# Optimization experiments

Hardware: AMD Instinct MI355X
Metric: run time of the kernel (lower is better)

## Reference

```python
import jax, jax.numpy as jnp
import numpy as np

RADIUS = 0.2
NSAMPLE = 32


def setup_inputs() -> dict:
    key = jax.random.key(0)
    k1, k2 = jax.random.split(key)
    B, N = 8, 4096
    xyz = jax.random.uniform(k1, (B, N, 3), dtype=jnp.float32)
    xyz_new = jax.random.uniform(k2, (B, N, 3), dtype=jnp.float32)  # ignored by forward, kept for signature fidelity
    return {"xyz": xyz, "xyz_new": xyz_new}


def _ball_query(radius, nsample, xyz, new_xyz):
    # xyz: [B, N, 3] source points; new_xyz: [B, M, 3] query centers.
    # Returns idx: [B, M, nsample] int32, matching pointnet2 CUDA ball_query:
    # first `nsample` indices j (in increasing j order) with ||q - p_j||^2 < r^2;
    # unused slots are filled with the first valid index.
    B, N, _ = xyz.shape
    sq_src = jnp.sum(xyz * xyz, axis=-1)          # [B, N]
    sq_q = jnp.sum(new_xyz * new_xyz, axis=-1)    # [B, M]
    # d2[b, m, n] = ||q_m - p_n||^2
    d2 = sq_q[:, :, None] + sq_src[:, None, :] - 2.0 * jnp.einsum(
        "bmc,bnc->bmn", new_xyz, xyz)             # [B, M, N]
    mask = d2 < (radius * radius)                 # [B, M, N] bool
    # key = index j when within radius, else sentinel N (sorts to the end)
    idx_range = jnp.arange(N, dtype=jnp.int32)
    keys = jnp.where(mask, idx_range[None, None, :], jnp.int32(N))
    sorted_keys = jnp.sort(keys, axis=-1)[..., :nsample]  # [B, M, nsample]
    first = sorted_keys[..., 0:1]                 # first valid index (pad value)
    idx = jnp.where(sorted_keys < N, sorted_keys, first)
    return idx.astype(jnp.int32)


def reference(xyz, xyz_new):
    # Faithful to the module: ball_query(radius, nsample, xyz, xyz) — xyz_new unused.
    return _ball_query(RADIUS, NSAMPLE, xyz, xyz)
```

## Files before the change

kernel.cpp:

```cpp
#include <hip/hip_runtime.h>
#include <cstdint>


#define BQ_N    4096
#define BQ_HALF 2048
#define BQ_B    8
#define BQ_NS   32
#define BQ_R2   0.04f

__device__ __forceinline__ float sq_plain(float x, float y, float z) {
    float r, t;
    asm("v_mul_f32 %0, %2, %2\n\t"
        "v_mul_f32 %1, %3, %3\n\t"
        "v_add_f32 %0, %0, %1\n\t"
        "v_mul_f32 %1, %4, %4\n\t"
        "v_add_f32 %0, %0, %1"
        : "=&v"(r), "=&v"(t)
        : "v"(x), "v"(y), "v"(z));
    return r;
}

__device__ __forceinline__ float d2_mixed(float qx, float qy, float qz, float sqq,
                                          float sx, float sy, float sz, float sqs) {
    float r, t;
    asm("v_mul_f32 %0, %2, %5\n\t"
        "v_fma_f32 %0, %3, %6, %0\n\t"
        "v_fma_f32 %0, %4, %7, %0\n\t"
        "v_add_f32 %0, %0, %0\n\t"
        "v_add_f32 %1, %8, %9\n\t"
        "v_sub_f32 %0, %1, %0"
        : "=&v"(r), "=&v"(t)
        : "v"(qx), "v"(qy), "v"(qz), "v"(sx), "v"(sy), "v"(sz),
          "v"(sqq), "v"(sqs));
    return r;
}

__device__ __forceinline__ void scan1(const float4* pts, int lane,
                                      const float4& q, int c,
                                      uint64_t& word, int& found) {
    #pragma unroll
    for (int u = 0; u < 4; ++u) {
        const int k = (c << 2) + u;
        const float4 s = pts[((k & 31) << 6) + lane];
        const float d2 = d2_mixed(q.x, q.y, q.z, q.w, s.x, s.y, s.z, s.w);
        const uint64_t bal = __ballot(d2 < BQ_R2);
        if (lane == k) word = bal;
        found += (int)__popcll(bal);
    }
}

__device__ __forceinline__ void scan2(const float4* pts, int lane,
                                      const float4& q0, const float4& q1,
                                      int c0, int c1,
                                      uint64_t& w0, uint64_t& w1,
                                      int& f0, int& f1) {
    int c = c0;
    while (c < c1) {
        #pragma unroll
        for (int u = 0; u < 4; ++u) {
            const int k = (c << 2) + u;
            const float4 s = pts[((k & 31) << 6) + lane];
            const float d20 = d2_mixed(q0.x, q0.y, q0.z, q0.w,
                                       s.x, s.y, s.z, s.w);
            const float d21 = d2_mixed(q1.x, q1.y, q1.z, q1.w,
                                       s.x, s.y, s.z, s.w);
            const uint64_t b0 = __ballot(d20 < BQ_R2);
            const uint64_t b1 = __ballot(d21 < BQ_R2);
            if (lane == k) { w0 = b0; w1 = b1; }
            f0 += (int)__popcll(b0);
            f1 += (int)__popcll(b1);
        }
        ++c;
        if (f0 >= BQ_NS || f1 >= BQ_NS) break;
    }
    for (int ca = c; ca < c1 && f0 < BQ_NS; ++ca) scan1(pts, lane, q0, ca, w0, f0);
    for (int cb = c; cb < c1 && f1 < BQ_NS; ++cb) scan1(pts, lane, q1, cb, w1, f1);
}

__device__ __forceinline__ void emit_query(int* orow, int lane, uint64_t word) {
    const int cnt = __popcll(word);
    int incl = cnt;
    #pragma unroll
    for (int off = 1; off < 64; off <<= 1) {
        const int t = __shfl_up(incl, off);
        if (lane >= off) incl += t;
    }
    const int pre   = incl - cnt;
    const int total = __shfl(incl, 63);

    int first;
    const uint64_t nz = __ballot(word != 0ull);
    if (nz == 0ull) {
        first = BQ_N;
    } else {
        const int fl = __builtin_ctzll(nz);
        const uint64_t fw = __shfl(word, fl);
        first = (fl << 6) + __builtin_ctzll(fw);
    }

    uint64_t w = word;
    int pos = pre;
    while (w != 0ull && pos < BQ_NS) {
        const int bit = __builtin_ctzll(w);
        orow[pos] = (lane << 6) + bit;
        w &= (w - 1);
        ++pos;
    }
    if (lane >= total && lane < BQ_NS) orow[lane] = first;
}

__global__ __launch_bounds__(256, 4)
void ball_query_kernel(const float* __restrict__ xyz, int* __restrict__ out)
{
    __shared__ float4 pts[BQ_HALF];

    const int b     = blockIdx.x >> 7;
    const int qbase = (blockIdx.x & 127) << 5;
    const float* __restrict__ src = xyz + (size_t)b * BQ_N * 3;
    const int lane = threadIdx.x & 63;
    const int wid  = threadIdx.x >> 6;
    int* __restrict__ outb = out + (size_t)(b * BQ_N) * BQ_NS;

    float4 Q[8];
    #pragma unroll
    for (int j = 0; j < 8; ++j) {
        const int m = qbase + (wid << 3) + j;
        const float x = src[3 * m + 0];
        const float y = src[3 * m + 1];
        const float z = src[3 * m + 2];
        Q[j] = make_float4(x, y, z, sq_plain(x, y, z));
    }

    for (int j = threadIdx.x; j < BQ_HALF; j += 256) {
        const float x = src[3 * j + 0];
        const float y = src[3 * j + 1];
        const float z = src[3 * j + 2];
        pts[j] = make_float4(x, y, z, sq_plain(x, y, z));
    }
    __syncthreads();

    uint64_t W[8] = {0, 0, 0, 0, 0, 0, 0, 0};
    int      F[8] = {0, 0, 0, 0, 0, 0, 0, 0};

    #pragma unroll
    for (int p = 0; p < 4; ++p)
        scan2(pts, lane, Q[p], Q[p + 4], 0, 8, W[p], W[p + 4], F[p], F[p + 4]);

    __syncthreads();
    for (int j = threadIdx.x; j < BQ_HALF; j += 256) {
        const int g = BQ_HALF + j;
        const float x = src[3 * g + 0];
        const float y = src[3 * g + 1];
        const float z = src[3 * g + 2];
        pts[j] = make_float4(x, y, z, sq_plain(x, y, z));
    }
    __syncthreads();

    #pragma unroll
    for (int p = 0; p < 4; ++p) {
        if (F[p] < BQ_NS && F[p + 4] < BQ_NS) {
            scan2(pts, lane, Q[p], Q[p + 4], 8, 16,
                  W[p], W[p + 4], F[p], F[p + 4]);
        } else if (F[p] < BQ_NS) {
            for (int ca = 8; ca < 16 && F[p] < BQ_NS; ++ca)
                scan1(pts, lane, Q[p], ca, W[p], F[p]);
        } else if (F[p + 4] < BQ_NS) {
            for (int cb = 8; cb < 16 && F[p + 4] < BQ_NS; ++cb)
                scan1(pts, lane, Q[p + 4], cb, W[p + 4], F[p + 4]);
        }
    }

    #pragma unroll
    for (int j = 0; j < 8; ++j) {
        const int m = qbase + (wid << 3) + j;
        emit_query(outb + (size_t)m * BQ_NS, lane, W[j]);
    }
}

extern "C" void kernel_launch(void* const* d_in, const int* in_sizes, int n_in,
                              void* d_out, int out_size, void* d_ws, size_t ws_size,
                              hipStream_t stream)
{
    const float* xyz = (const float*)d_in[0];
    int* out = (int*)d_out;
    hipLaunchKernelGGL(ball_query_kernel, dim3(1024), dim3(256), 0, stream,
                       xyz, out);
}
```

Measured before the change: 83.71 us.

## Stream source points from global memory and drop shared-memory staging

The shared-memory staging of source points, with its two-phase load and block barriers, is removed. Each wave now reads xyz directly from global memory (relying on L1/L2 caching) and computes squared norms on the fly. Blocks shrink to 128 threads with 4 queries per wave, so more blocks launch. Per-lane prefix counts are recorded during the scan, which removes the shuffle-based prefix sum in emit, and the pad value is computed only when fewer than nsample neighbours were found. The trade-off is strided 3-float global loads and recomputing norms per query pair instead of loading them once into LDS.

```diff
diff --git a/kernel.cpp b/kernel.cpp
--- a/kernel.cpp
+++ b/kernel.cpp
@@ -3,7 +3,6 @@
 
 
 #define BQ_N    4096
-#define BQ_HALF 2048
 #define BQ_B    8
 #define BQ_NS   32
 #define BQ_R2   0.04f
@@ -35,145 +34,117 @@
     return r;
 }
 
-__device__ __forceinline__ void scan1(const float4* pts, int lane,
-                                      const float4& q, int c,
-                                      uint64_t& word, int& found) {
+__device__ __forceinline__ void scan1g(const float* __restrict__ src, int lane,
+                                       const float4& q, int c,
+                                       uint64_t& word, int& wpre, int& found) {
+    float X[4], Y[4], Z[4];
     #pragma unroll
     for (int u = 0; u < 4; ++u) {
         const int k = (c << 2) + u;
-        const float4 s = pts[((k & 31) << 6) + lane];
-        const float d2 = d2_mixed(q.x, q.y, q.z, q.w, s.x, s.y, s.z, s.w);
+        const float* ptr = src + (size_t)(((k << 6) + lane) * 3);
+        X[u] = ptr[0]; Y[u] = ptr[1]; Z[u] = ptr[2];
+    }
+    #pragma unroll
+    for (int u = 0; u < 4; ++u) {
+        const int k = (c << 2) + u;
+        const float sqs = sq_plain(X[u], Y[u], Z[u]);
+        const float d2  = d2_mixed(q.x, q.y, q.z, q.w, X[u], Y[u], Z[u], sqs);
         const uint64_t bal = __ballot(d2 < BQ_R2);
-        if (lane == k) word = bal;
+        if (lane == k) { word = bal; wpre = found; }
         found += (int)__popcll(bal);
     }
 }
 
-__device__ __forceinline__ void scan2(const float4* pts, int lane,
-                                      const float4& q0, const float4& q1,
-                                      int c0, int c1,
-                                      uint64_t& w0, uint64_t& w1,
-                                      int& f0, int& f1) {
+__device__ __forceinline__ void scan2g(const float* __restrict__ src, int lane,
+                                       const float4& q0, const float4& q1,
+                                       int c0, int c1,
+                                       uint64_t& w0, uint64_t& w1,
+                                       int& p0, int& p1, int& f0, int& f1) {
     int c = c0;
     while (c < c1) {
+        float X[4], Y[4], Z[4];
         #pragma unroll
         for (int u = 0; u < 4; ++u) {
             const int k = (c << 2) + u;
-            const float4 s = pts[((k & 31) << 6) + lane];
+            const float* ptr = src + (size_t)(((k << 6) + lane) * 3);
+            X[u] = ptr[0]; Y[u] = ptr[1]; Z[u] = ptr[2];
+        }
+        #pragma unroll
+        for (int u = 0; u < 4; ++u) {
+            const int k = (c << 2) + u;
+            const float sqs = sq_plain(X[u], Y[u], Z[u]);
             const float d20 = d2_mixed(q0.x, q0.y, q0.z, q0.w,
-                                       s.x, s.y, s.z, s.w);
+                                       X[u], Y[u], Z[u], sqs);
             const float d21 = d2_mixed(q1.x, q1.y, q1.z, q1.w,
-                                       s.x, s.y, s.z, s.w);
+                                       X[u], Y[u], Z[u], sqs);
             const uint64_t b0 = __ballot(d20 < BQ_R2);
             const uint64_t b1 = __ballot(d21 < BQ_R2);
-            if (lane == k) { w0 = b0; w1 = b1; }
+            if (lane == k) { w0 = b0; w1 = b1; p0 = f0; p1 = f1; }
             f0 += (int)__popcll(b0);
             f1 += (int)__popcll(b1);
         }
         ++c;
         if (f0 >= BQ_NS || f1 >= BQ_NS) break;
     }
-    for (int ca = c; ca < c1 && f0 < BQ_NS; ++ca) scan1(pts, lane, q0, ca, w0, f0);
-    for (int cb = c; cb < c1 && f1 < BQ_NS; ++cb) scan1(pts, lane, q1, cb, w1, f1);
+    for (int ca = c; ca < c1 && f0 < BQ_NS; ++ca) scan1g(src, lane, q0, ca, w0, p0, f0);
+    for (int cb = c; cb < c1 && f1 < BQ_NS; ++cb) scan1g(src, lane, q1, cb, w1, p1, f1);
 }
 
-__device__ __forceinline__ void emit_query(int* orow, int lane, uint64_t word) {
-    const int cnt = __popcll(word);
-    int incl = cnt;
-    #pragma unroll
-    for (int off = 1; off < 64; off <<= 1) {
-        const int t = __shfl_up(incl, off);
-        if (lane >= off) incl += t;
-    }
-    const int pre   = incl - cnt;
-    const int total = __shfl(incl, 63);
-
-    int first;
-    const uint64_t nz = __ballot(word != 0ull);
-    if (nz == 0ull) {
-        first = BQ_N;
-    } else {
-        const int fl = __builtin_ctzll(nz);
-        const uint64_t fw = __shfl(word, fl);
-        first = (fl << 6) + __builtin_ctzll(fw);
-    }
-
+__device__ __forceinline__ void emit_query(int* __restrict__ orow, int lane,
+                                           uint64_t word, int wpre, int total) {
     uint64_t w = word;
-    int pos = pre;
+    int pos = wpre;
     while (w != 0ull && pos < BQ_NS) {
         const int bit = __builtin_ctzll(w);
         orow[pos] = (lane << 6) + bit;
         w &= (w - 1);
         ++pos;
     }
-    if (lane >= total && lane < BQ_NS) orow[lane] = first;
+    if (total < BQ_NS) {
+        int first;
+        const uint64_t nz = __ballot(word != 0ull);
+        if (nz == 0ull) {
+            first = BQ_N;
+        } else {
+            const int fl = __builtin_ctzll(nz);
+            const uint64_t fw = __shfl(word, fl);
+            first = (fl << 6) + __builtin_ctzll(fw);
+        }
+        if (lane >= total && lane < BQ_NS) orow[lane] = first;
+    }
 }
 
-__global__ __launch_bounds__(256, 4)
+__global__ __launch_bounds__(128, 4)
 void ball_query_kernel(const float* __restrict__ xyz, int* __restrict__ out)
 {
-    __shared__ float4 pts[BQ_HALF];
-
-    const int b     = blockIdx.x >> 7;
-    const int qbase = (blockIdx.x & 127) << 5;
+    const int b     = blockIdx.x >> 9;
+    const int qbase = (blockIdx.x & 511) << 3;
+    const int lane  = threadIdx.x & 63;
+    const int wid   = threadIdx.x >> 6;
     const float* __restrict__ src = xyz + (size_t)b * BQ_N * 3;
-    const int lane = threadIdx.x & 63;
-    const int wid  = threadIdx.x >> 6;
     int* __restrict__ outb = out + (size_t)(b * BQ_N) * BQ_NS;
 
-    float4 Q[8];
+    float4 Q[4];
     #pragma unroll
-    for (int j = 0; j < 8; ++j) {
-        const int m = qbase + (wid << 3) + j;
+    for (int j = 0; j < 4; ++j) {
+        const int m = qbase + (wid << 2) + j;
         const float x = src[3 * m + 0];
         const float y = src[3 * m + 1];
         const float z = src[3 * m + 2];
         Q[j] = make_float4(x, y, z, sq_plain(x, y, z));
     }
 
-    for (int j = threadIdx.x; j < BQ_HALF; j += 256) {
-        const float x = src[3 * j + 0];
-        const float y = src[3 * j + 1];
-        const float z = src[3 * j + 2];
-        pts[j] = make_float4(x, y, z, sq_plain(x, y, z));
-    }
-    __syncthreads();
+    uint64_t W[4] = {0, 0, 0, 0};
+    int      P[4] = {0, 0, 0, 0};
+    int      F[4] = {0, 0, 0, 0};
 
-    uint64_t W[8] = {0, 0, 0, 0, 0, 0, 0, 0};
-    int      F[8] = {0, 0, 0, 0, 0, 0, 0, 0};
+    scan2g(src, lane, Q[0], Q[1], 0, 16, W[0], W[1], P[0], P[1], F[0], F[1]);
+    scan2g(src, lane, Q[2], Q[3], 0, 16, W[2], W[3], P[2], P[3], F[2], F[3]);
 
     #pragma unroll
-    for (int p = 0; p < 4; ++p)
-        scan2(pts, lane, Q[p], Q[p + 4], 0, 8, W[p], W[p + 4], F[p], F[p + 4]);
-
-    __syncthreads();
-    for (int j = threadIdx.x; j < BQ_HALF; j += 256) {
-        const int g = BQ_HALF + j;
-        const float x = src[3 * g + 0];
-        const float y = src[3 * g + 1];
-        const float z = src[3 * g + 2];
-        pts[j] = make_float4(x, y, z, sq_plain(x, y, z));
-    }
-    __syncthreads();
-
-    #pragma unroll
-    for (int p = 0; p < 4; ++p) {
-        if (F[p] < BQ_NS && F[p + 4] < BQ_NS) {
-            scan2(pts, lane, Q[p], Q[p + 4], 8, 16,
-                  W[p], W[p + 4], F[p], F[p + 4]);
-        } else if (F[p] < BQ_NS) {
-            for (int ca = 8; ca < 16 && F[p] < BQ_NS; ++ca)
-                scan1(pts, lane, Q[p], ca, W[p], F[p]);
-        } else if (F[p + 4] < BQ_NS) {
-            for (int cb = 8; cb < 16 && F[p + 4] < BQ_NS; ++cb)
-                scan1(pts, lane, Q[p + 4], cb, W[p + 4], F[p + 4]);
-        }
-    }
-
-    #pragma unroll
-    for (int j = 0; j < 8; ++j) {
-        const int m = qbase + (wid << 3) + j;
-        emit_query(outb + (size_t)m * BQ_NS, lane, W[j]);
+    for (int j = 0; j < 4; ++j) {
+        const int m = qbase + (wid << 2) + j;
+        emit_query(outb + (size_t)m * BQ_NS, lane, W[j], P[j], F[j]);
     }
 }
 
@@ -183,6 +154,6 @@
 {
     const float* xyz = (const float*)d_in[0];
     int* out = (int*)d_out;
-    hipLaunchKernelGGL(ball_query_kernel, dim3(1024), dim3(256), 0, stream,
+    hipLaunchKernelGGL(ball_query_kernel, dim3(4096), dim3(128), 0, stream,
                        xyz, out);
 }
```

Result: faster. 79.09 us (-5.5%).
